# Performance work log

Hardware: AMD Instinct MI355X
Metric: run time of the kernel (lower is better)

The kernel has to match this reference:

```python
import jax, jax.numpy as jnp
import numpy as np

DIM = 1024
HEADS = 16
HEAD_DIM = DIM // HEADS
B, N = 2, 2048


def setup_inputs() -> dict:
    key = jax.random.key(0)
    k1, k2, k3, k4 = jax.random.split(key, 4)
    x = jax.random.normal(k1, (B, N, DIM), dtype=jnp.float32)
    # torch Linear weights: shape (out_features, in_features), y = x @ W.T + b
    w_qkv = jax.random.normal(k2, (3 * DIM, DIM), dtype=jnp.float32) * (DIM ** -0.5)
    w_proj = jax.random.normal(k3, (DIM, DIM), dtype=jnp.float32) * (DIM ** -0.5)
    b_proj = jax.random.normal(k4, (DIM,), dtype=jnp.float32) * 0.01
    return {"x": x, "w_qkv": w_qkv, "w_proj": w_proj, "b_proj": b_proj}


def reference(x, w_qkv, w_proj, b_proj):
    Bb, Nn, D = x.shape
    scale = HEAD_DIM ** -0.5
    qkv = x @ w_qkv.T                                # [B, N, 3D]
    qkv = qkv.reshape(Bb, Nn, 3, HEADS, HEAD_DIM)
    qkv = jnp.transpose(qkv, (2, 0, 3, 1, 4))        # [3, B, H, N, hd]
    q, k, v = qkv[0], qkv[1], qkv[2]
    attn = jnp.einsum('bhqd,bhkd->bhqk', q, k) * scale
    attn = jax.nn.softmax(attn, axis=-1)
    out = jnp.einsum('bhqk,bhkd->bhqd', attn, v)     # [B, H, N, hd]
    out = jnp.transpose(out, (0, 2, 1, 3)).reshape(Bb, Nn, D)
    return out @ w_proj.T + b_proj
```

## Files before the change

### kernel.cpp

```cpp
#include <hip/hip_runtime.h>
#include <hip/hip_bf16.h>
#include <cstdint>
#include <cstddef>

using u16 = unsigned short;
using u32 = uint32_t;
using f32x4  = __attribute__((ext_vector_type(4))) float;
using bf16x8 = __attribute__((ext_vector_type(8))) __bf16;
using s16x4  = __attribute__((ext_vector_type(4))) short;

#define D_MODEL 1024
#define N_HEADS 16
#define HD      64
#define SEQ     2048
#define QKV_LD  3072
#define K2SCALE 0.18033688011112042f

__device__ __forceinline__ u16 f2b(float f) {
  union { float f; u32 u; } v; v.f = f;
  u32 r = 0x7FFFu + ((v.u >> 16) & 1u);
  return (u16)((v.u + r) >> 16);
}

__device__ __forceinline__ u32 pkbf16(float a, float b) {
  union { __hip_bfloat162 h; u32 u; } c;
  c.h = __float22bfloat162_rn(float2{a, b});
  return c.u;
}

#define MFMA16(A, B, C) __builtin_amdgcn_mfma_f32_16x16x16bf16_1k(A, B, C, 0, 0, 0)

__device__ __forceinline__ void gld16(const u16* g, u16* l) {
  __builtin_amdgcn_global_load_lds(
      (const __attribute__((address_space(1))) void*)g,
      (__attribute__((address_space(3))) void*)l, 16, 0, 0);
}

__global__ void cast3_bf16(const float* __restrict__ x, const float* __restrict__ wq,
                           const float* __restrict__ wp, u16* __restrict__ dst) {
  int i = blockIdx.x * blockDim.x + threadIdx.x;
  const float* src;
  int off;
  if (blockIdx.x < 4096)      { src = x;  off = 0; }
  else if (blockIdx.x < 7168) { src = wq; off = 4096 * 256; }
  else                        { src = wp; off = 7168 * 256; }
  float4 f = ((const float4*)src)[i - off];
  u32 lo = pkbf16(f.x, f.y), hi = pkbf16(f.z, f.w);
  uint2 o = {lo, hi};
  ((uint2*)dst)[i] = o;
}

template<int OUTMODE, int MT>
__launch_bounds__(256, 3)
__global__ void gemm_nt(const u16* __restrict__ A, const u16* __restrict__ B,
                        u16* __restrict__ Ob, float* __restrict__ Of,
                        const float* __restrict__ bias, int N, int K) {
  __shared__ __attribute__((aligned(16))) u16 sA[2][MT * 32];
  __shared__ __attribute__((aligned(16))) u16 sB[2][128 * 32];

  const int tid  = threadIdx.x;
  const int lane = tid & 63;
  const int w    = tid >> 6;
  const int qd   = lane >> 4;
  const int ln   = lane & 15;
  constexpr int MI = MT / 32;
  const int wm   = (w >> 1) * (MT / 2);
  const int wn   = (w & 1) * 64;
  const int m0   = blockIdx.y * MT;
  const int n0   = blockIdx.x * 128;

  auto stage = [&](int kk, int buf) {
    int k0 = kk * 32;
    #pragma unroll
    for (int c = 0; c < MT / 64; ++c) {
      int sbase = w * MT + c * 64;
      int s = sbase + lane;
      int line = s >> 3, sub = (s & 7) ^ (line & 7);
      int row = line * 2 + (sub >> 2), col = (sub & 3) * 8;
      gld16(A + (size_t)(m0 + row) * K + k0 + col, &sA[buf][sbase * 8]);
    }
    #pragma unroll
    for (int c = 0; c < 2; ++c) {
      int sbase = w * 128 + c * 64;
      int s = sbase + lane;
      int line = s >> 3, sub = (s & 7) ^ (line & 7);
      int row = line * 2 + (sub >> 2), col = (sub & 3) * 8;
      gld16(B + (size_t)(n0 + row) * K + k0 + col, &sB[buf][sbase * 8]);
    }
  };

  f32x4 acc[MI][4] = {};
  const int NK = K >> 5;
  stage(0, 0);

  for (int kk = 0; kk < NK; ++kk) {
    const int cur = kk & 1;
    __syncthreads();
    if (kk + 1 < NK) stage(kk + 1, cur ^ 1);

    bf16x8 af[MI], bfm[4];
    #pragma unroll
    for (int i = 0; i < MI; ++i) {
      int r = wm + i * 16 + ln;
      af[i] = *(const bf16x8*)&sA[cur][(r >> 1) * 64 +
                ((((r & 1) << 5) + qd * 8) ^ (((r >> 1) & 7) << 3))];
    }
    #pragma unroll
    for (int j = 0; j < 4; ++j) {
      int r = wn + j * 16 + ln;
      bfm[j] = *(const bf16x8*)&sB[cur][(r >> 1) * 64 +
                ((((r & 1) << 5) + qd * 8) ^ (((r >> 1) & 7) << 3))];
    }
    #pragma unroll
    for (int i = 0; i < MI; ++i)
      #pragma unroll
      for (int j = 0; j < 4; ++j)
        acc[i][j] = __builtin_amdgcn_mfma_f32_16x16x32_bf16(af[i], bfm[j], acc[i][j], 0, 0, 0);
  }

  #pragma unroll
  for (int i = 0; i < MI; ++i) {
    #pragma unroll
    for (int j = 0; j < 4; ++j) {
      #pragma unroll
      for (int r = 0; r < 4; ++r) {
        int row = m0 + wm + i * 16 + qd * 4 + r;
        int col = n0 + wn + j * 16 + ln;
        float v = acc[i][j][r];
        if (OUTMODE == 0) {
          if (col < D_MODEL) v *= K2SCALE;
          Ob[(size_t)row * N + col] = f2b(v);
        } else {
          Of[(size_t)row * N + col] = v + bias[col];
        }
      }
    }
  }
}

__launch_bounds__(256, 3)
__global__ void attn_kernel(const u16* __restrict__ qkv, u16* __restrict__ outb) {
  __shared__ __attribute__((aligned(16))) u16 smem[16384];
  u16 (*sK)[64 * 64] = (u16(*)[64 * 64])smem;
  u32 (*sVT)[64 * 32]   = (u32(*)[64 * 32])(smem + 8192);

  const int tid  = threadIdx.x;
  const int lane = tid & 63;
  const int w    = tid >> 6;
  const int qd   = lane >> 4;
  const int ln   = lane & 15;
  const int qp   = blockIdx.x;
  const int h    = blockIdx.y & 15;
  const int b    = blockIdx.y >> 4;
  const size_t tokbase = (size_t)b * SEQ;
  const int q0   = qp * 128;
  const int qoff = h * HD;
  const int koff = D_MODEL + h * HD;
  const int voff = 2 * D_MODEL + h * HD;

  bf16x8 aq[2][2];
  #pragma unroll
  for (int c2 = 0; c2 < 2; ++c2)
    #pragma unroll
    for (int hf = 0; hf < 2; ++hf)
      aq[c2][hf] = *(const bf16x8*)(qkv + (tokbase + q0 + c2 * 64 + w * 16 + ln) * QKV_LD
                                    + qoff + hf * 32 + qd * 8);

  auto stageK = [&](int kt, int buf) {
    #pragma unroll
    for (int c = 0; c < 2; ++c) {
      int sbase = c * 256 + w * 64;
      int s = sbase + lane;
      int row = s >> 3, sub = (s & 7) ^ (row & 7);
      gld16(qkv + (tokbase + kt * 64 + row) * QKV_LD + koff + sub * 8,
            &sK[buf][sbase * 8]);
    }
  };
  auto loadV = [&](int kt, uint4& va, uint4& vb) {
    int tp = tid & 31, d0 = (tid >> 5) * 8;
    const u16* g0 = qkv + (tokbase + kt * 64 + tp * 2) * QKV_LD + voff + d0;
    va = *(const uint4*)g0;
    vb = *(const uint4*)(g0 + QKV_LD);
  };
  auto writeV = [&](int buf, const uint4& va, const uint4& vb) {
    int tp = tid & 31, d0 = (tid >> 5) * 8;
    const u32* a  = (const u32*)&va;
    const u32* bb = (const u32*)&vb;
    #pragma unroll
    for (int e = 0; e < 4; ++e) {
      sVT[buf][(d0 + 2 * e    ) * 32 + (tp ^ (e << 3)    )] =
          __builtin_amdgcn_perm(bb[e], a[e], 0x05040100u);
      sVT[buf][(d0 + 2 * e + 1) * 32 + (tp ^ (e << 3) ^ 4)] =
          __builtin_amdgcn_perm(bb[e], a[e], 0x07060302u);
    }
  };

  stageK(0, 0);
  uint4 va, vb;
  loadV(0, va, vb);
  writeV(0, va, vb);
  loadV(1, va, vb);

  f32x4 accOT[2][4] = {};
  float psum[2] = {0.f, 0.f};
  const int tsw = (ln & 7) << 2;
  const int ksw = (ln & 7) << 3;

  for (int kt = 0; kt < 32; ++kt) {
    const int cur = kt & 1, nxt = cur ^ 1;
    __syncthreads();
    if (kt < 31) { stageK(kt + 1, nxt); writeV(nxt, va, vb); }
    if (kt < 30) { loadV(kt + 2, va, vb); }

    #pragma unroll
    for (int cb = 0; cb < 4; ++cb) {
      bf16x8 ak0 = *(const bf16x8*)&sK[cur][(cb * 16 + ln) * 64 + ((qd * 8) ^ ksw)];
      bf16x8 ak1 = *(const bf16x8*)&sK[cur][(cb * 16 + ln) * 64 + ((32 + qd * 8) ^ ksw)];
      f32x4 st[2];
      #pragma unroll
      for (int c2 = 0; c2 < 2; ++c2) {
        f32x4 z = {0.f, 0.f, 0.f, 0.f};
        f32x4 t = __builtin_amdgcn_mfma_f32_16x16x32_bf16(ak0, aq[c2][0], z, 0, 0, 0);
        st[c2]  = __builtin_amdgcn_mfma_f32_16x16x32_bf16(ak1, aq[c2][1], t, 0, 0, 0);
      }
      s16x4 pf[2];
      #pragma unroll
      for (int c2 = 0; c2 < 2; ++c2) {
        float p0 = __builtin_amdgcn_exp2f(st[c2][0]);
        float p1 = __builtin_amdgcn_exp2f(st[c2][1]);
        float p2 = __builtin_amdgcn_exp2f(st[c2][2]);
        float p3 = __builtin_amdgcn_exp2f(st[c2][3]);
        psum[c2] += (p0 + p1) + (p2 + p3);
        union { u32 d[2]; s16x4 v; } pk;
        pk.d[0] = pkbf16(p0, p1);
        pk.d[1] = pkbf16(p2, p3);
        pf[c2] = pk.v;
      }
      #pragma unroll
      for (int ob = 0; ob < 4; ++ob) {
        s16x4 vf = *(const s16x4*)&sVT[cur][(ob * 16 + ln) * 32
                                           + ((cb * 8 + qd * 2) ^ tsw)];
        accOT[0][ob] = MFMA16(vf, pf[0], accOT[0][ob]);
        accOT[1][ob] = MFMA16(vf, pf[1], accOT[1][ob]);
      }
    }
  }

  #pragma unroll
  for (int c2 = 0; c2 < 2; ++c2) {
    float s = psum[c2];
    s += __shfl_xor(s, 16, 64);
    s += __shfl_xor(s, 32, 64);
    psum[c2] = 1.0f / s;
  }

  u16* sOut = smem;
  __syncthreads();
  #pragma unroll
  for (int c2 = 0; c2 < 2; ++c2)
    #pragma unroll
    for (int ob = 0; ob < 4; ++ob) {
      u32 lo = pkbf16(accOT[c2][ob][0] * psum[c2], accOT[c2][ob][1] * psum[c2]);
      u32 hi = pkbf16(accOT[c2][ob][2] * psum[c2], accOT[c2][ob][3] * psum[c2]);
      ((u32*)sOut)[(c2 * 64 + w * 16 + ln) * 36 + ob * 8 + qd * 2    ] = lo;
      ((u32*)sOut)[(c2 * 64 + w * 16 + ln) * 36 + ob * 8 + qd * 2 + 1] = hi;
    }
  __syncthreads();
  #pragma unroll
  for (int it = 0; it < 4; ++it) {
    int idx = it * 256 + tid;
    int token = idx >> 3, chunk = idx & 7;
    uint4 v = *(const uint4*)&sOut[token * 72 + chunk * 8];
    *(uint4*)&outb[(tokbase + q0 + token) * D_MODEL + h * HD + chunk * 8] = v;
  }
}

extern "C" void kernel_launch(void* const* d_in, const int* in_sizes, int n_in,
                              void* d_out, int out_size, void* d_ws, size_t ws_size,
                              hipStream_t stream) {
  const float* x      = (const float*)d_in[0];
  const float* w_qkv  = (const float*)d_in[1];
  const float* w_proj = (const float*)d_in[2];
  const float* b_proj = (const float*)d_in[3];
  float* out = (float*)d_out;

  u16* ws     = (u16*)d_ws;
  u16* xb     = ws;
  u16* wqkvb  = xb    + (size_t)4096 * 1024;
  u16* wprojb = wqkvb + (size_t)3072 * 1024;
  u16* qkvb   = wprojb + (size_t)1024 * 1024;
  u16* attnb  = qkvb  + (size_t)4096 * 3072;

  cast3_bf16<<<8192, 256, 0, stream>>>(x, w_qkv, w_proj, xb);

  gemm_nt<0, 128><<<dim3(24, 32), 256, 0, stream>>>(xb, wqkvb, qkvb, nullptr, nullptr, 3072, 1024);

  attn_kernel<<<dim3(16, 32), 256, 0, stream>>>(qkvb, attnb);

  gemm_nt<1, 64><<<dim3(8, 64), 256, 0, stream>>>(attnb, wprojb, nullptr, out, b_proj, 1024, 1024);
}
```

Measured before the change: 182.7 us.

## Use 512-thread attention blocks with one 16-query tile per wave

Doubles the attention block to 8 waves so each wave handles a single 16-row query tile instead of two. K/V staging is split across twice as many threads, and the per-wave accumulator and softmax-sum state are halved. The aim is lower register pressure and more waves in flight to hide latency. The cost is that each K/V fragment read from LDS now feeds half as many MFMAs, so LDS traffic per unit of compute goes up, and each barrier now has to synchronise more waves.

```diff
diff --git a/kernel.cpp b/kernel.cpp
--- a/kernel.cpp
+++ b/kernel.cpp
@@ -138,7 +138,7 @@
   }
 }
 
-__launch_bounds__(256, 3)
+__launch_bounds__(512, 4)
 __global__ void attn_kernel(const u16* __restrict__ qkv, u16* __restrict__ outb) {
   __shared__ __attribute__((aligned(16))) u16 smem[16384];
   u16 (*sK)[64 * 64] = (u16(*)[64 * 64])smem;
@@ -158,51 +158,49 @@
   const int koff = D_MODEL + h * HD;
   const int voff = 2 * D_MODEL + h * HD;
 
-  bf16x8 aq[2][2];
-  #pragma unroll
-  for (int c2 = 0; c2 < 2; ++c2)
-    #pragma unroll
-    for (int hf = 0; hf < 2; ++hf)
-      aq[c2][hf] = *(const bf16x8*)(qkv + (tokbase + q0 + c2 * 64 + w * 16 + ln) * QKV_LD
-                                    + qoff + hf * 32 + qd * 8);
+  bf16x8 aq[2];
+  #pragma unroll
+  for (int hf = 0; hf < 2; ++hf)
+    aq[hf] = *(const bf16x8*)(qkv + (tokbase + q0 + w * 16 + ln) * QKV_LD
+                              + qoff + hf * 32 + qd * 8);
 
   auto stageK = [&](int kt, int buf) {
-    #pragma unroll
-    for (int c = 0; c < 2; ++c) {
-      int sbase = c * 256 + w * 64;
-      int s = sbase + lane;
-      int row = s >> 3, sub = (s & 7) ^ (row & 7);
-      gld16(qkv + (tokbase + kt * 64 + row) * QKV_LD + koff + sub * 8,
-            &sK[buf][sbase * 8]);
-    }
-  };
-  auto loadV = [&](int kt, uint4& va, uint4& vb) {
-    int tp = tid & 31, d0 = (tid >> 5) * 8;
-    const u16* g0 = qkv + (tokbase + kt * 64 + tp * 2) * QKV_LD + voff + d0;
-    va = *(const uint4*)g0;
-    vb = *(const uint4*)(g0 + QKV_LD);
-  };
-  auto writeV = [&](int buf, const uint4& va, const uint4& vb) {
-    int tp = tid & 31, d0 = (tid >> 5) * 8;
+    int sbase = w * 64;
+    int s = sbase + lane;
+    int row = s >> 3, sub = (s & 7) ^ (row & 7);
+    gld16(qkv + (tokbase + kt * 64 + row) * QKV_LD + koff + sub * 8,
+          &sK[buf][sbase * 8]);
+  };
+  auto loadV = [&](int kt, uint2& va, uint2& vb) {
+    int tp = tid & 31, dg = (tid >> 5) & 7, half = tid >> 8;
+    const u16* g0 = qkv + (tokbase + kt * 64 + tp * 2) * QKV_LD + voff
+                    + dg * 8 + half * 4;
+    va = *(const uint2*)g0;
+    vb = *(const uint2*)(g0 + QKV_LD);
+  };
+  auto writeV = [&](int buf, const uint2& va, const uint2& vb) {
+    int tp = tid & 31, dg = (tid >> 5) & 7, half = tid >> 8;
     const u32* a  = (const u32*)&va;
     const u32* bb = (const u32*)&vb;
     #pragma unroll
-    for (int e = 0; e < 4; ++e) {
-      sVT[buf][(d0 + 2 * e    ) * 32 + (tp ^ (e << 3)    )] =
-          __builtin_amdgcn_perm(bb[e], a[e], 0x05040100u);
-      sVT[buf][(d0 + 2 * e + 1) * 32 + (tp ^ (e << 3) ^ 4)] =
-          __builtin_amdgcn_perm(bb[e], a[e], 0x07060302u);
+    for (int e2 = 0; e2 < 2; ++e2) {
+      int e = half * 2 + e2;
+      int d = dg * 8 + 2 * e;
+      sVT[buf][(d    ) * 32 + (tp ^ (e << 3)    )] =
+          __builtin_amdgcn_perm(bb[e2], a[e2], 0x05040100u);
+      sVT[buf][(d + 1) * 32 + (tp ^ (e << 3) ^ 4)] =
+          __builtin_amdgcn_perm(bb[e2], a[e2], 0x07060302u);
     }
   };
 
   stageK(0, 0);
-  uint4 va, vb;
+  uint2 va, vb;
   loadV(0, va, vb);
   writeV(0, va, vb);
   loadV(1, va, vb);
 
-  f32x4 accOT[2][4] = {};
-  float psum[2] = {0.f, 0.f};
+  f32x4 accOT[4] = {};
+  float psum = 0.f;
   const int tsw = (ln & 7) << 2;
   const int ksw = (ln & 7) << 3;
 
@@ -216,59 +214,47 @@
     for (int cb = 0; cb < 4; ++cb) {
       bf16x8 ak0 = *(const bf16x8*)&sK[cur][(cb * 16 + ln) * 64 + ((qd * 8) ^ ksw)];
       bf16x8 ak1 = *(const bf16x8*)&sK[cur][(cb * 16 + ln) * 64 + ((32 + qd * 8) ^ ksw)];
-      f32x4 st[2];
-      #pragma unroll
-      for (int c2 = 0; c2 < 2; ++c2) {
-        f32x4 z = {0.f, 0.f, 0.f, 0.f};
-        f32x4 t = __builtin_amdgcn_mfma_f32_16x16x32_bf16(ak0, aq[c2][0], z, 0, 0, 0);
-        st[c2]  = __builtin_amdgcn_mfma_f32_16x16x32_bf16(ak1, aq[c2][1], t, 0, 0, 0);
-      }
-      s16x4 pf[2];
-      #pragma unroll
-      for (int c2 = 0; c2 < 2; ++c2) {
-        float p0 = __builtin_amdgcn_exp2f(st[c2][0]);
-        float p1 = __builtin_amdgcn_exp2f(st[c2][1]);
-        float p2 = __builtin_amdgcn_exp2f(st[c2][2]);
-        float p3 = __builtin_amdgcn_exp2f(st[c2][3]);
-        psum[c2] += (p0 + p1) + (p2 + p3);
-        union { u32 d[2]; s16x4 v; } pk;
-        pk.d[0] = pkbf16(p0, p1);
-        pk.d[1] = pkbf16(p2, p3);
-        pf[c2] = pk.v;
-      }
+      f32x4 z = {0.f, 0.f, 0.f, 0.f};
+      f32x4 t  = __builtin_amdgcn_mfma_f32_16x16x32_bf16(ak0, aq[0], z, 0, 0, 0);
+      f32x4 st = __builtin_amdgcn_mfma_f32_16x16x32_bf16(ak1, aq[1], t, 0, 0, 0);
+
+      float p0 = __builtin_amdgcn_exp2f(st[0]);
+      float p1 = __builtin_amdgcn_exp2f(st[1]);
+      float p2 = __builtin_amdgcn_exp2f(st[2]);
+      float p3 = __builtin_amdgcn_exp2f(st[3]);
+      psum += (p0 + p1) + (p2 + p3);
+      union { u32 d[2]; s16x4 v; } pk;
+      pk.d[0] = pkbf16(p0, p1);
+      pk.d[1] = pkbf16(p2, p3);
+      s16x4 pf = pk.v;
+
       #pragma unroll
       for (int ob = 0; ob < 4; ++ob) {
         s16x4 vf = *(const s16x4*)&sVT[cur][(ob * 16 + ln) * 32
                                            + ((cb * 8 + qd * 2) ^ tsw)];
-        accOT[0][ob] = MFMA16(vf, pf[0], accOT[0][ob]);
-        accOT[1][ob] = MFMA16(vf, pf[1], accOT[1][ob]);
+        accOT[ob] = MFMA16(vf, pf, accOT[ob]);
       }
     }
   }
 
-  #pragma unroll
-  for (int c2 = 0; c2 < 2; ++c2) {
-    float s = psum[c2];
-    s += __shfl_xor(s, 16, 64);
-    s += __shfl_xor(s, 32, 64);
-    psum[c2] = 1.0f / s;
-  }
+  float s = psum;
+  s += __shfl_xor(s, 16, 64);
+  s += __shfl_xor(s, 32, 64);
+  const float pinv = 1.0f / s;
 
   u16* sOut = smem;
   __syncthreads();
   #pragma unroll
-  for (int c2 = 0; c2 < 2; ++c2)
-    #pragma unroll
-    for (int ob = 0; ob < 4; ++ob) {
-      u32 lo = pkbf16(accOT[c2][ob][0] * psum[c2], accOT[c2][ob][1] * psum[c2]);
-      u32 hi = pkbf16(accOT[c2][ob][2] * psum[c2], accOT[c2][ob][3] * psum[c2]);
-      ((u32*)sOut)[(c2 * 64 + w * 16 + ln) * 36 + ob * 8 + qd * 2    ] = lo;
-      ((u32*)sOut)[(c2 * 64 + w * 16 + ln) * 36 + ob * 8 + qd * 2 + 1] = hi;
-    }
+  for (int ob = 0; ob < 4; ++ob) {
+    u32 lo = pkbf16(accOT[ob][0] * pinv, accOT[ob][1] * pinv);
+    u32 hi = pkbf16(accOT[ob][2] * pinv, accOT[ob][3] * pinv);
+    ((u32*)sOut)[(w * 16 + ln) * 36 + ob * 8 + qd * 2    ] = lo;
+    ((u32*)sOut)[(w * 16 + ln) * 36 + ob * 8 + qd * 2 + 1] = hi;
+  }
   __syncthreads();
   #pragma unroll
-  for (int it = 0; it < 4; ++it) {
-    int idx = it * 256 + tid;
+  for (int it = 0; it < 2; ++it) {
+    int idx = it * 512 + tid;
     int token = idx >> 3, chunk = idx & 7;
     uint4 v = *(const uint4*)&sOut[token * 72 + chunk * 8];
     *(uint4*)&outb[(tokbase + q0 + token) * D_MODEL + h * HD + chunk * 8] = v;
@@ -295,7 +281,7 @@
 
   gemm_nt<0, 128><<<dim3(24, 32), 256, 0, stream>>>(xb, wqkvb, qkvb, nullptr, nullptr, 3072, 1024);
 
-  attn_kernel<<<dim3(16, 32), 256, 0, stream>>>(qkvb, attnb);
+  attn_kernel<<<dim3(16, 32), 512, 0, stream>>>(qkvb, attnb);
 
   gemm_nt<1, 64><<<dim3(8, 64), 256, 0, stream>>>(attnb, wprojb, nullptr, out, b_proj, 1024, 1024);
 }
```

New measurement: 193.8 us. 1.06x slower.

## Split key tiles across two wave groups in attention with shared-memory reduction

Applied to the files above, without the earlier changes.

The attention block grows from 256 to 512 threads. Two groups of four waves each handle half of the 16-row key chunks of every 64-key tile, and K/V staging is spread across all threads. Partial softmax row sums and partial P·V accumulators are then combined through shared memory before the bf16 output is written. The aim is more waves in flight per block to hide MFMA and exp latency. The cost is extra LDS traffic, extra barriers in the epilogue, and register pressure under the tighter launch bounds.

```diff
diff --git a/kernel.cpp b/kernel.cpp
--- a/kernel.cpp
+++ b/kernel.cpp
@@ -138,15 +138,17 @@
   }
 }
 
-__launch_bounds__(256, 3)
+__launch_bounds__(512, 4)
 __global__ void attn_kernel(const u16* __restrict__ qkv, u16* __restrict__ outb) {
-  __shared__ __attribute__((aligned(16))) u16 smem[16384];
+  __shared__ __attribute__((aligned(16))) u16 smem[18432];
   u16 (*sK)[64 * 64] = (u16(*)[64 * 64])smem;
   u32 (*sVT)[64 * 32]   = (u32(*)[64 * 32])(smem + 8192);
 
   const int tid  = threadIdx.x;
   const int lane = tid & 63;
   const int w    = tid >> 6;
+  const int g    = w >> 2;
+  const int wg   = w & 3;
   const int qd   = lane >> 4;
   const int ln   = lane & 15;
   const int qp   = blockIdx.x;
@@ -163,40 +165,40 @@
   for (int c2 = 0; c2 < 2; ++c2)
     #pragma unroll
     for (int hf = 0; hf < 2; ++hf)
-      aq[c2][hf] = *(const bf16x8*)(qkv + (tokbase + q0 + c2 * 64 + w * 16 + ln) * QKV_LD
+      aq[c2][hf] = *(const bf16x8*)(qkv + (tokbase + q0 + c2 * 64 + wg * 16 + ln) * QKV_LD
                                     + qoff + hf * 32 + qd * 8);
 
   auto stageK = [&](int kt, int buf) {
-    #pragma unroll
-    for (int c = 0; c < 2; ++c) {
-      int sbase = c * 256 + w * 64;
-      int s = sbase + lane;
-      int row = s >> 3, sub = (s & 7) ^ (row & 7);
-      gld16(qkv + (tokbase + kt * 64 + row) * QKV_LD + koff + sub * 8,
-            &sK[buf][sbase * 8]);
-    }
+    int sbase = w * 64;
+    int s = sbase + lane;
+    int row = s >> 3, sub = (s & 7) ^ (row & 7);
+    gld16(qkv + (tokbase + kt * 64 + row) * QKV_LD + koff + sub * 8,
+          &sK[buf][sbase * 8]);
   };
-  auto loadV = [&](int kt, uint4& va, uint4& vb) {
-    int tp = tid & 31, d0 = (tid >> 5) * 8;
-    const u16* g0 = qkv + (tokbase + kt * 64 + tp * 2) * QKV_LD + voff + d0;
-    va = *(const uint4*)g0;
-    vb = *(const uint4*)(g0 + QKV_LD);
+  auto loadV = [&](int kt, uint2& va, uint2& vb) {
+    int tp = tid & 31, dg = (tid >> 5) & 7, half = tid >> 8;
+    const u16* g0 = qkv + (tokbase + kt * 64 + tp * 2) * QKV_LD + voff
+                    + dg * 8 + half * 4;
+    va = *(const uint2*)g0;
+    vb = *(const uint2*)(g0 + QKV_LD);
   };
-  auto writeV = [&](int buf, const uint4& va, const uint4& vb) {
-    int tp = tid & 31, d0 = (tid >> 5) * 8;
+  auto writeV = [&](int buf, const uint2& va, const uint2& vb) {
+    int tp = tid & 31, dg = (tid >> 5) & 7, half = tid >> 8;
     const u32* a  = (const u32*)&va;
     const u32* bb = (const u32*)&vb;
     #pragma unroll
-    for (int e = 0; e < 4; ++e) {
-      sVT[buf][(d0 + 2 * e    ) * 32 + (tp ^ (e << 3)    )] =
-          __builtin_amdgcn_perm(bb[e], a[e], 0x05040100u);
-      sVT[buf][(d0 + 2 * e + 1) * 32 + (tp ^ (e << 3) ^ 4)] =
-          __builtin_amdgcn_perm(bb[e], a[e], 0x07060302u);
+    for (int e2 = 0; e2 < 2; ++e2) {
+      int e = half * 2 + e2;
+      int d = dg * 8 + 2 * e;
+      sVT[buf][(d    ) * 32 + (tp ^ (e << 3)    )] =
+          __builtin_amdgcn_perm(bb[e2], a[e2], 0x05040100u);
+      sVT[buf][(d + 1) * 32 + (tp ^ (e << 3) ^ 4)] =
+          __builtin_amdgcn_perm(bb[e2], a[e2], 0x07060302u);
     }
   };
 
   stageK(0, 0);
-  uint4 va, vb;
+  uint2 va, vb;
   loadV(0, va, vb);
   writeV(0, va, vb);
   loadV(1, va, vb);
@@ -213,7 +215,8 @@
     if (kt < 30) { loadV(kt + 2, va, vb); }
 
     #pragma unroll
-    for (int cb = 0; cb < 4; ++cb) {
+    for (int cbi = 0; cbi < 2; ++cbi) {
+      const int cb = g * 2 + cbi;
       bf16x8 ak0 = *(const bf16x8*)&sK[cur][(cb * 16 + ln) * 64 + ((qd * 8) ^ ksw)];
       bf16x8 ak1 = *(const bf16x8*)&sK[cur][(cb * 16 + ln) * 64 + ((32 + qd * 8) ^ ksw)];
       f32x4 st[2];
@@ -246,32 +249,63 @@
     }
   }
 
+  float ps[2];
   #pragma unroll
   for (int c2 = 0; c2 < 2; ++c2) {
     float s = psum[c2];
     s += __shfl_xor(s, 16, 64);
     s += __shfl_xor(s, 32, 64);
-    psum[c2] = 1.0f / s;
-  }
-
-  u16* sOut = smem;
-  __syncthreads();
+    ps[c2] = s;
+  }
+
+  float* sPs = (float*)(smem + 17408);
+  __syncthreads();
+  if (qd == 0) {
+    sPs[((g * 2 + 0) * 4 + wg) * 16 + ln] = ps[0];
+    sPs[((g * 2 + 1) * 4 + wg) * 16 + ln] = ps[1];
+  }
+  __syncthreads();
+  float pinv[2];
   #pragma unroll
-  for (int c2 = 0; c2 < 2; ++c2)
-    #pragma unroll
-    for (int ob = 0; ob < 4; ++ob) {
-      u32 lo = pkbf16(accOT[c2][ob][0] * psum[c2], accOT[c2][ob][1] * psum[c2]);
-      u32 hi = pkbf16(accOT[c2][ob][2] * psum[c2], accOT[c2][ob][3] * psum[c2]);
-      ((u32*)sOut)[(c2 * 64 + w * 16 + ln) * 36 + ob * 8 + qd * 2    ] = lo;
-      ((u32*)sOut)[(c2 * 64 + w * 16 + ln) * 36 + ob * 8 + qd * 2 + 1] = hi;
-    }
-  __syncthreads();
-  #pragma unroll
-  for (int it = 0; it < 4; ++it) {
-    int idx = it * 256 + tid;
-    int token = idx >> 3, chunk = idx & 7;
-    uint4 v = *(const uint4*)&sOut[token * 72 + chunk * 8];
-    *(uint4*)&outb[(tokbase + q0 + token) * D_MODEL + h * HD + chunk * 8] = v;
+  for (int c2 = 0; c2 < 2; ++c2) {
+    float other = sPs[(((1 - g) * 2 + c2) * 4 + wg) * 16 + ln];
+    pinv[c2] = 1.0f / (ps[c2] + other);
+  }
+
+  float* sAcc = (float*)smem;
+  __syncthreads();
+  if (g == 0) {
+    #pragma unroll
+    for (int c2 = 0; c2 < 2; ++c2)
+      #pragma unroll
+      for (int ob = 0; ob < 4; ++ob) {
+        f32x4 t = accOT[c2][ob] * pinv[c2];
+        *(f32x4*)&sAcc[(c2 * 64 + wg * 16 + ln) * 72 + ob * 16 + qd * 4] = t;
+      }
+  }
+  __syncthreads();
+  if (g == 1) {
+    #pragma unroll
+    for (int c2 = 0; c2 < 2; ++c2)
+      #pragma unroll
+      for (int ob = 0; ob < 4; ++ob) {
+        float* p = &sAcc[(c2 * 64 + wg * 16 + ln) * 72 + ob * 16 + qd * 4];
+        f32x4 t = *(const f32x4*)p;
+        t += accOT[c2][ob] * pinv[c2];
+        *(f32x4*)p = t;
+      }
+  }
+  __syncthreads();
+
+  {
+    int token = tid >> 2, seg = tid & 3;
+    const float* src = &sAcc[token * 72 + seg * 16];
+    u32 o[8];
+    #pragma unroll
+    for (int e = 0; e < 8; ++e) o[e] = pkbf16(src[2 * e], src[2 * e + 1]);
+    u16* dst = &outb[(tokbase + q0 + token) * D_MODEL + h * HD + seg * 16];
+    *(uint4*)dst       = *(uint4*)&o[0];
+    *(uint4*)(dst + 8) = *(uint4*)&o[4];
   }
 }
 
@@ -295,7 +329,7 @@
 
   gemm_nt<0, 128><<<dim3(24, 32), 256, 0, stream>>>(xb, wqkvb, qkvb, nullptr, nullptr, 3072, 1024);
 
-  attn_kernel<<<dim3(16, 32), 256, 0, stream>>>(qkvb, attnb);
+  attn_kernel<<<dim3(16, 32), 512, 0, stream>>>(qkvb, attnb);
 
   gemm_nt<1, 64><<<dim3(8, 64), 256, 0, stream>>>(attnb, wprojb, nullptr, out, b_proj, 1024, 1024);
 }
```

After: 196.2 us. 7.4% more time.

## Software-pipeline attention QK and PV across tiles, swizzle GEMM block order

Applied to the files above, without the earlier changes.

The attention loop is restructured so the QK^T MFMAs for tile t+1 are issued before the exp/PV work for tile t. This uses ping-pong score registers and a triple-buffered transposed-V shared buffer, so the two MFMA chains can overlap with the exp work. Occupancy hint drops from 3 to 2 blocks per CU because of the extra registers and LDS. The GEMM kernel also remaps block indices with an 8-way swizzle, which changes which tiles run together and is meant to improve cache locality across concurrent blocks.

```diff
diff --git a/kernel.cpp b/kernel.cpp
--- a/kernel.cpp
+++ b/kernel.cpp
@@ -66,8 +66,13 @@
   constexpr int MI = MT / 32;
   const int wm   = (w >> 1) * (MT / 2);
   const int wn   = (w & 1) * 64;
-  const int m0   = blockIdx.y * MT;
-  const int n0   = blockIdx.x * 128;
+
+  const int nbx = gridDim.x;
+  const int lin = blockIdx.y * nbx + blockIdx.x;
+  const int cpx = (nbx * gridDim.y) >> 3;
+  const int swz = (lin & 7) * cpx + (lin >> 3);
+  const int m0  = (swz / nbx) * MT;
+  const int n0  = (swz % nbx) * 128;
 
   auto stage = [&](int kk, int buf) {
     int k0 = kk * 32;
@@ -138,11 +143,13 @@
   }
 }
 
-__launch_bounds__(256, 3)
+__launch_bounds__(256, 2)
 __global__ void attn_kernel(const u16* __restrict__ qkv, u16* __restrict__ outb) {
-  __shared__ __attribute__((aligned(16))) u16 smem[16384];
+  __shared__ __attribute__((aligned(16))) u16 smem[20480];
   u16 (*sK)[64 * 64] = (u16(*)[64 * 64])smem;
-  u32 (*sVT)[64 * 32]   = (u32(*)[64 * 32])(smem + 8192);
+  u32* const sVT0 = (u32*)(smem + 8192);
+  u32* const sVT1 = sVT0 + 64 * 32;
+  u32* const sVT2 = sVT1 + 64 * 32;
 
   const int tid  = threadIdx.x;
   const int lane = tid & 63;
@@ -182,54 +189,49 @@
     va = *(const uint4*)g0;
     vb = *(const uint4*)(g0 + QKV_LD);
   };
-  auto writeV = [&](int buf, const uint4& va, const uint4& vb) {
+  auto writeV = [&](u32* vbuf, const uint4& va, const uint4& vb) {
     int tp = tid & 31, d0 = (tid >> 5) * 8;
     const u32* a  = (const u32*)&va;
     const u32* bb = (const u32*)&vb;
     #pragma unroll
     for (int e = 0; e < 4; ++e) {
-      sVT[buf][(d0 + 2 * e    ) * 32 + (tp ^ (e << 3)    )] =
+      vbuf[(d0 + 2 * e    ) * 32 + (tp ^ (e << 3)    )] =
           __builtin_amdgcn_perm(bb[e], a[e], 0x05040100u);
-      sVT[buf][(d0 + 2 * e + 1) * 32 + (tp ^ (e << 3) ^ 4)] =
+      vbuf[(d0 + 2 * e + 1) * 32 + (tp ^ (e << 3) ^ 4)] =
           __builtin_amdgcn_perm(bb[e], a[e], 0x07060302u);
     }
   };
 
-  stageK(0, 0);
-  uint4 va, vb;
-  loadV(0, va, vb);
-  writeV(0, va, vb);
-  loadV(1, va, vb);
-
   f32x4 accOT[2][4] = {};
+  f32x4 stA[4][2], stB[4][2];
   float psum[2] = {0.f, 0.f};
   const int tsw = (ln & 7) << 2;
   const int ksw = (ln & 7) << 3;
 
-  for (int kt = 0; kt < 32; ++kt) {
-    const int cur = kt & 1, nxt = cur ^ 1;
-    __syncthreads();
-    if (kt < 31) { stageK(kt + 1, nxt); writeV(nxt, va, vb); }
-    if (kt < 30) { loadV(kt + 2, va, vb); }
-
+  auto qk_phase = [&](int t, f32x4 (&stW)[4][2]) {
+    const int cur = t & 1;
     #pragma unroll
     for (int cb = 0; cb < 4; ++cb) {
       bf16x8 ak0 = *(const bf16x8*)&sK[cur][(cb * 16 + ln) * 64 + ((qd * 8) ^ ksw)];
       bf16x8 ak1 = *(const bf16x8*)&sK[cur][(cb * 16 + ln) * 64 + ((32 + qd * 8) ^ ksw)];
-      f32x4 st[2];
       #pragma unroll
       for (int c2 = 0; c2 < 2; ++c2) {
         f32x4 z = {0.f, 0.f, 0.f, 0.f};
-        f32x4 t = __builtin_amdgcn_mfma_f32_16x16x32_bf16(ak0, aq[c2][0], z, 0, 0, 0);
-        st[c2]  = __builtin_amdgcn_mfma_f32_16x16x32_bf16(ak1, aq[c2][1], t, 0, 0, 0);
+        f32x4 t0 = __builtin_amdgcn_mfma_f32_16x16x32_bf16(ak0, aq[c2][0], z, 0, 0, 0);
+        stW[cb][c2] = __builtin_amdgcn_mfma_f32_16x16x32_bf16(ak1, aq[c2][1], t0, 0, 0, 0);
       }
+    }
+  };
+  auto fin_phase = [&](f32x4 (&stR)[4][2], const u32* vP) {
+    #pragma unroll
+    for (int cb = 0; cb < 4; ++cb) {
       s16x4 pf[2];
       #pragma unroll
       for (int c2 = 0; c2 < 2; ++c2) {
-        float p0 = __builtin_amdgcn_exp2f(st[c2][0]);
-        float p1 = __builtin_amdgcn_exp2f(st[c2][1]);
-        float p2 = __builtin_amdgcn_exp2f(st[c2][2]);
-        float p3 = __builtin_amdgcn_exp2f(st[c2][3]);
+        float p0 = __builtin_amdgcn_exp2f(stR[cb][c2][0]);
+        float p1 = __builtin_amdgcn_exp2f(stR[cb][c2][1]);
+        float p2 = __builtin_amdgcn_exp2f(stR[cb][c2][2]);
+        float p3 = __builtin_amdgcn_exp2f(stR[cb][c2][3]);
         psum[c2] += (p0 + p1) + (p2 + p3);
         union { u32 d[2]; s16x4 v; } pk;
         pk.d[0] = pkbf16(p0, p1);
@@ -238,13 +240,50 @@
       }
       #pragma unroll
       for (int ob = 0; ob < 4; ++ob) {
-        s16x4 vf = *(const s16x4*)&sVT[cur][(ob * 16 + ln) * 32
-                                           + ((cb * 8 + qd * 2) ^ tsw)];
+        s16x4 vf = *(const s16x4*)&vP[(ob * 16 + ln) * 32 + ((cb * 8 + qd * 2) ^ tsw)];
         accOT[0][ob] = MFMA16(vf, pf[0], accOT[0][ob]);
         accOT[1][ob] = MFMA16(vf, pf[1], accOT[1][ob]);
       }
     }
-  }
+  };
+
+  stageK(0, 0);
+  uint4 va, vb;
+  loadV(0, va, vb);
+  writeV(sVT0, va, vb);
+  loadV(1, va, vb);
+  u32 *vPrev = sVT2, *vCur = sVT0, *vNext = sVT1;
+
+  __syncthreads();
+  stageK(1, 1);
+  writeV(vNext, va, vb);
+  loadV(2, va, vb);
+  qk_phase(0, stA);
+  { u32* t = vPrev; vPrev = vCur; vCur = vNext; vNext = t; }
+
+  for (int S = 0; S < 15; ++S) {
+    const int t1 = 2 * S + 1;
+    __syncthreads();
+    stageK(t1 + 1, (t1 + 1) & 1);
+    writeV(vNext, va, vb);
+    loadV(t1 + 2, va, vb);
+    qk_phase(t1, stB);
+    fin_phase(stA, vPrev);
+    { u32* t = vPrev; vPrev = vCur; vCur = vNext; vNext = t; }
+    const int t2 = t1 + 1;
+    __syncthreads();
+    stageK(t2 + 1, (t2 + 1) & 1);
+    writeV(vNext, va, vb);
+    if (t2 < 30) loadV(t2 + 2, va, vb);
+    qk_phase(t2, stA);
+    fin_phase(stB, vPrev);
+    { u32* t = vPrev; vPrev = vCur; vCur = vNext; vNext = t; }
+  }
+
+  __syncthreads();
+  qk_phase(31, stB);
+  fin_phase(stA, vPrev);
+  fin_phase(stB, vCur);
 
   #pragma unroll
   for (int c2 = 0; c2 < 2; ++c2) {
```

Result: no change. 182.6 us (-0.0%).
